# Optimization experiments

Measured on AMD Instinct MI355X. Metric: run time of the kernel, lower is better.

## Reference

```python
import jax, jax.numpy as jnp
import numpy as np

N_NODES = 100000
N_EDGES = 1600000
D_IN = 128
D_HID = 128
N_LAYERS = 3


def setup_inputs() -> dict:
    key = jax.random.key(0)
    ks = jax.random.split(key, 7)
    x = jax.random.normal(ks[0], (N_NODES, D_IN), dtype=jnp.float32)
    edge_index = jax.random.randint(ks[1], (2, N_EDGES), 0, N_NODES, dtype=jnp.int32)
    s = 1.0 / np.sqrt(D_HID)
    # stacked per-layer MLP params: lin1 (in->h), lin2 (h->h); in==h==128 for all layers
    W1 = jax.random.uniform(ks[2], (N_LAYERS, D_IN, D_HID), jnp.float32, -s, s)
    b1 = jax.random.uniform(ks[3], (N_LAYERS, D_HID), jnp.float32, -s, s)
    W2 = jax.random.uniform(ks[4], (N_LAYERS, D_HID, D_HID), jnp.float32, -s, s)
    b2 = jax.random.uniform(ks[5], (N_LAYERS, D_HID), jnp.float32, -s, s)
    return {"x": x, "edge_index": edge_index, "W1": W1, "b1": b1, "W2": W2, "b2": b2}


def _gin_layer(x, src, dst, W1, b1, W2, b2):
    # GINConv: out = MLP((1+eps)*x + sum_{j in N(i)} x_j), eps = 0
    agg = jax.ops.segment_sum(x[src], dst, num_segments=N_NODES)  # [N, C]
    h = x + agg
    h = jnp.maximum(h @ W1 + b1, 0.0)  # MLP internal ReLU
    return h @ W2 + b2


def reference(x, edge_index, W1, b1, W2, b2):
    src, dst = edge_index[0], edge_index[1]
    for i in range(N_LAYERS):
        x = _gin_layer(x, src, dst, W1[i], b1[i], W2[i], b2[i])
        if i < N_LAYERS - 1:  # inter-layer act (norm=Identity, dropout=0)
            x = jnp.maximum(x, 0.0)
    return x
```

## Files before the change

kernel.cpp:

```cpp
#include <hip/hip_runtime.h>
#include <hip/hip_bf16.h>

#define D 128
#define DD (128 * 128)

typedef float f32x4 __attribute__((ext_vector_type(4)));
typedef __bf16 bf16x8 __attribute__((ext_vector_type(8)));

__device__ __forceinline__ unsigned short f2bf(float f) {
  unsigned int u = __float_as_uint(f);
  u += 0x7fff + ((u >> 16) & 1);
  return (unsigned short)(u >> 16);
}

__device__ __forceinline__ void gl_lds16(const void* g, void* l) {
  __builtin_amdgcn_global_load_lds(
      (const __attribute__((address_space(1))) unsigned int*)g,
      (__attribute__((address_space(3))) unsigned int*)l, 16, 0, 0);
}

__device__ __forceinline__ int wave_incl_scan(int v, int lane) {
#pragma unroll
  for (int d = 1; d < 64; d <<= 1) {
    int t = __shfl_up(v, d);
    if (lane >= d) v += t;
  }
  return v;
}

#define NBK 196
#define CHUNK 4096

__global__ __launch_bounds__(256) void k_bhistP(const int* __restrict__ dst, int E,
                                                int* __restrict__ bcount, int CBn,
                                                const float* __restrict__ W1,
                                                const float* __restrict__ W2,
                                                unsigned short* __restrict__ Wt) {
  __shared__ int cnt[NBK];
  if ((int)blockIdx.x >= CBn) {
    int b = (int)blockIdx.x - CBn;
    const float* W = (b & 1) ? (W2 + (size_t)(b >> 1) * DD) : (W1 + (size_t)(b >> 1) * DD);
    unsigned short* O = Wt + (size_t)b * DD;
    for (int i = threadIdx.x; i < DD; i += 256) {
      int n = i >> 7, k = i & 127;
      O[n * D + k] = f2bf(W[k * D + n]);
    }
    return;
  }
  const int tid = threadIdx.x;
  for (int i = tid; i < NBK; i += 256) cnt[i] = 0;
  __syncthreads();
  const int e0 = blockIdx.x * CHUNK;
  const int emax = min(e0 + CHUNK, E);
  for (int e = e0 + tid; e < emax; e += 256)
    atomicAdd(&cnt[((unsigned)dst[e]) >> 9], 1);
  __syncthreads();
  for (int i = tid; i < NBK; i += 256)
    if (cnt[i]) atomicAdd(&bcount[i], cnt[i]);
}

__global__ __launch_bounds__(256) void k_binA(const int* __restrict__ src,
                                              const int* __restrict__ dst, int E,
                                              const int* __restrict__ bcount,
                                              int* __restrict__ bcursor,
                                              int* __restrict__ pairbuf) {
  __shared__ int cnt[NBK];
  __shared__ int base[NBK];
  __shared__ int bb[NBK];
  __shared__ int ws4[4];
  const int tid = threadIdx.x;
  const int e0 = blockIdx.x * CHUNK;
  const int emax = min(e0 + CHUNK, E);
  for (int i = tid; i < NBK; i += 256) cnt[i] = 0;
  {
    int lane = tid & 63, w = tid >> 6;
    int v = (tid < NBK) ? bcount[tid] : 0;
    int s = wave_incl_scan(v, lane);
    if (lane == 63) ws4[w] = s;
    __syncthreads();
    if (tid < NBK) {
      int off = 0;
      for (int k = 0; k < w; k++) off += ws4[k];
      bb[tid] = off + s - v;
    }
  }
  __syncthreads();
  for (int e = e0 + tid; e < emax; e += 256)
    atomicAdd(&cnt[((unsigned)dst[e]) >> 9], 1);
  __syncthreads();
  for (int i = tid; i < NBK; i += 256) {
    int c = cnt[i];
    int b = 0;
    if (c) b = atomicAdd(&bcursor[i], c) + bb[i];
    base[i] = b;
    cnt[i] = 0;
  }
  __syncthreads();
  for (int e = e0 + tid; e < emax; e += 256) {
    int d = dst[e];
    int bk = ((unsigned)d) >> 9;
    int pos = base[bk] + atomicAdd(&cnt[bk], 1);
    pairbuf[pos] = (src[e] << 9) | (d & 511);
  }
}

#define SEG_CAP 12800
__global__ __launch_bounds__(256) void k_binB(const int* __restrict__ pairbuf,
                                              const int* __restrict__ bcount,
                                              int* __restrict__ col,
                                              int* __restrict__ row_ptr, int N) {
  __shared__ int sdeg[512];
  __shared__ int rpl[512];
  __shared__ int cur[512];
  __shared__ int wsum[4];
  __shared__ int wsum2[4];
  __shared__ int stage[SEG_CAP];
  const int tid = threadIdx.x;
  const int lane = tid & 63, wid = tid >> 6;
  const int node0 = blockIdx.x << 9;
  const int nn = min(512, N - node0);
  {
    int vv = (tid < (int)blockIdx.x) ? bcount[tid] : 0;
    vv += __shfl_down(vv, 32); vv += __shfl_down(vv, 16);
    vv += __shfl_down(vv, 8);  vv += __shfl_down(vv, 4);
    vv += __shfl_down(vv, 2);  vv += __shfl_down(vv, 1);
    if (lane == 0) wsum2[wid] = vv;
  }
  for (int i = tid; i < 512; i += 256) { sdeg[i] = 0; cur[i] = 0; }
  __syncthreads();
  const int start = wsum2[0] + wsum2[1] + wsum2[2] + wsum2[3];
  const int end = start + bcount[blockIdx.x];
  const int sz = end - start;
  for (int i = tid; i < sz; i += 256)
    atomicAdd(&sdeg[pairbuf[start + i] & 511], 1);
  __syncthreads();
  int a = sdeg[2 * tid], b = sdeg[2 * tid + 1];
  int v = a + b;
  int s = wave_incl_scan(v, lane);
  if (lane == 63) wsum[wid] = s;
  __syncthreads();
  int off = 0;
  for (int k = 0; k < wid; k++) off += wsum[k];
  int e0l = off + s - v;
  rpl[2 * tid] = e0l;
  rpl[2 * tid + 1] = e0l + a;
  __syncthreads();
  for (int i = tid; i < nn; i += 256) row_ptr[node0 + i] = start + rpl[i];
  if (blockIdx.x == gridDim.x - 1 && tid == 0) row_ptr[N] = end;
  for (int i = tid; i < sz; i += 256) {
    int pk = pairbuf[start + i];
    int d = pk & 511;
    int pos = rpl[d] + atomicAdd(&cur[d], 1);
    if (pos < SEG_CAP) stage[pos] = (int)(((unsigned)pk) >> 9);
  }
  __syncthreads();
  for (int i = tid; i < sz; i += 256) col[start + i] = stage[i];
}

__global__ __launch_bounds__(256) void k_agg(const unsigned short* __restrict__ Y,
                                             const int* __restrict__ row_ptr,
                                             const int* __restrict__ col,
                                             const float* __restrict__ bias,
                                             unsigned short* __restrict__ H, int N) {
  int wid = (blockIdx.x * 256 + threadIdx.x) >> 6;
  int lane = threadIdx.x & 63;
  if (wid >= N) return;
  const unsigned int* Yu = (const unsigned int*)Y;
  unsigned int sv = Yu[(size_t)wid * 64 + lane];
  float2 bv = ((const float2*)bias)[lane];
  float ax = bv.x + __uint_as_float(sv << 16);
  float ay = bv.y + __uint_as_float(sv & 0xffff0000u);
  int rs = row_ptr[wid], re = row_ptr[wid + 1];
  int dcap = min(re - rs, 64);
  int cv = (lane < dcap) ? col[rs + lane] : 0;
  int j = 0;
  for (; j + 8 <= dcap; j += 8) {
    int s0 = __shfl(cv, j + 0), s1 = __shfl(cv, j + 1);
    int s2 = __shfl(cv, j + 2), s3 = __shfl(cv, j + 3);
    int s4 = __shfl(cv, j + 4), s5 = __shfl(cv, j + 5);
    int s6 = __shfl(cv, j + 6), s7 = __shfl(cv, j + 7);
    unsigned int v0 = Yu[(size_t)s0 * 64 + lane];
    unsigned int v1 = Yu[(size_t)s1 * 64 + lane];
    unsigned int v2 = Yu[(size_t)s2 * 64 + lane];
    unsigned int v3 = Yu[(size_t)s3 * 64 + lane];
    unsigned int v4 = Yu[(size_t)s4 * 64 + lane];
    unsigned int v5 = Yu[(size_t)s5 * 64 + lane];
    unsigned int v6 = Yu[(size_t)s6 * 64 + lane];
    unsigned int v7 = Yu[(size_t)s7 * 64 + lane];
    ax += ((__uint_as_float(v0 << 16) + __uint_as_float(v1 << 16)) +
           (__uint_as_float(v2 << 16) + __uint_as_float(v3 << 16))) +
          ((__uint_as_float(v4 << 16) + __uint_as_float(v5 << 16)) +
           (__uint_as_float(v6 << 16) + __uint_as_float(v7 << 16)));
    ay += ((__uint_as_float(v0 & 0xffff0000u) + __uint_as_float(v1 & 0xffff0000u)) +
           (__uint_as_float(v2 & 0xffff0000u) + __uint_as_float(v3 & 0xffff0000u))) +
          ((__uint_as_float(v4 & 0xffff0000u) + __uint_as_float(v5 & 0xffff0000u)) +
           (__uint_as_float(v6 & 0xffff0000u) + __uint_as_float(v7 & 0xffff0000u)));
  }
  for (; j < dcap; j++) {
    int s = __shfl(cv, j);
    unsigned int v = Yu[(size_t)s * 64 + lane];
    ax += __uint_as_float(v << 16);
    ay += __uint_as_float(v & 0xffff0000u);
  }
  for (int t = rs + 64; t < re; t++) {
    unsigned int v = Yu[(size_t)col[t] * 64 + lane];
    ax += __uint_as_float(v << 16);
    ay += __uint_as_float(v & 0xffff0000u);
  }
  ax = fmaxf(ax, 0.f);
  ay = fmaxf(ay, 0.f);
  ((unsigned int*)H)[(size_t)wid * 64 + lane] =
      ((unsigned int)f2bf(ay) << 16) | f2bf(ax);
}

template <bool A_FP32, bool OUT_FP32>
__global__ __launch_bounds__(256) void k_gemm(const void* __restrict__ Ain,
                                              const unsigned short* __restrict__ Wt,
                                              const float* __restrict__ bias,
                                              void* __restrict__ Cout, int M, int relu) {
  __shared__ __align__(16) unsigned short As[64 * 128];
  __shared__ __align__(16) unsigned short Bs[128 * 128];
  const int tid = threadIdx.x;
  const int wid = tid >> 6, lane = tid & 63;
  const int R0 = blockIdx.x * 64;

#pragma unroll
  for (int g = 0; g < 8; g++) {
    int flat = g * 256 + tid;
    int n = flat >> 4, p = flat & 15;
    int l = p ^ (n & 15);
    gl_lds16(Wt + (size_t)n * D + l * 8, &Bs[(size_t)(g * 256 + wid * 64) * 8]);
  }
  if (A_FP32) {
    const float* A = (const float*)Ain;
#pragma unroll
    for (int g = 0; g < 4; g++) {
      int flat = g * 256 + tid;
      int row = flat >> 4, p = flat & 15;
      int l = p ^ (row & 15);
      float4 a0 = make_float4(0.f, 0.f, 0.f, 0.f), a1 = a0;
      if (R0 + row < M) {
        a0 = *(const float4*)(A + (size_t)(R0 + row) * D + l * 8);
        a1 = *(const float4*)(A + (size_t)(R0 + row) * D + l * 8 + 4);
      }
      ushort4 v0, v1;
      v0.x = f2bf(a0.x); v0.y = f2bf(a0.y); v0.z = f2bf(a0.z); v0.w = f2bf(a0.w);
      v1.x = f2bf(a1.x); v1.y = f2bf(a1.y); v1.z = f2bf(a1.z); v1.w = f2bf(a1.w);
      *(ushort4*)&As[row * D + p * 8] = v0;
      *(ushort4*)&As[row * D + p * 8 + 4] = v1;
    }
  } else {
    const unsigned short* A = (const unsigned short*)Ain;
#pragma unroll
    for (int g = 0; g < 4; g++) {
      int flat = g * 256 + tid;
      int row = flat >> 4, p = flat & 15;
      int l = p ^ (row & 15);
      gl_lds16(A + (size_t)(R0 + row) * D + l * 8, &As[(size_t)(g * 256 + wid * 64) * 8]);
    }
  }
  __syncthreads();

  const int wr = wid >> 1, wc = wid & 1;
  const int lm = lane & 15, lq = lane >> 4;
  f32x4 acc[2][4];
#pragma unroll
  for (int i = 0; i < 2; i++)
#pragma unroll
    for (int j = 0; j < 4; j++) acc[i][j] = f32x4{0.f, 0.f, 0.f, 0.f};

#pragma unroll
  for (int kc = 0; kc < 4; kc++) {
    const int pc = (kc * 4 + lq) ^ lm;
    bf16x8 af[2], bfr[4];
#pragma unroll
    for (int i = 0; i < 2; i++)
      af[i] = *(const bf16x8*)&As[(wr * 32 + i * 16 + lm) * D + pc * 8];
#pragma unroll
    for (int j = 0; j < 4; j++)
      bfr[j] = *(const bf16x8*)&Bs[(wc * 64 + j * 16 + lm) * D + pc * 8];
#pragma unroll
    for (int i = 0; i < 2; i++)
#pragma unroll
      for (int j = 0; j < 4; j++)
        acc[i][j] = __builtin_amdgcn_mfma_f32_16x16x32_bf16(af[i], bfr[j], acc[i][j], 0, 0, 0);
  }

  float bv[4];
#pragma unroll
  for (int j = 0; j < 4; j++) bv[j] = bias ? bias[wc * 64 + j * 16 + lm] : 0.f;
#pragma unroll
  for (int i = 0; i < 2; i++) {
#pragma unroll
    for (int reg = 0; reg < 4; reg++) {
      const int gr = R0 + wr * 32 + i * 16 + lq * 4 + reg;
      if (gr < M) {
#pragma unroll
        for (int j = 0; j < 4; j++) {
          const int gc = wc * 64 + j * 16 + lm;
          float v = acc[i][j][reg] + bv[j];
          if (relu) v = fmaxf(v, 0.f);
          if (OUT_FP32)
            ((float*)Cout)[(size_t)gr * D + gc] = v;
          else
            ((unsigned short*)Cout)[(size_t)gr * D + gc] = f2bf(v);
        }
      }
    }
  }
}

__global__ __launch_bounds__(256) void k_gemm2(const unsigned short* __restrict__ Ain,
                                               const unsigned short* __restrict__ W2t,
                                               const unsigned short* __restrict__ W1t,
                                               const float* __restrict__ b2,
                                               unsigned short* __restrict__ Cout, int M) {
  __shared__ __align__(16) unsigned short As[64 * 128];
  __shared__ __align__(16) unsigned short Bs[128 * 128];
  const int tid = threadIdx.x;
  const int wid = tid >> 6, lane = tid & 63;
  const int R0 = blockIdx.x * 64;

#pragma unroll
  for (int g = 0; g < 8; g++) {
    int flat = g * 256 + tid;
    int n = flat >> 4, p = flat & 15;
    int l = p ^ (n & 15);
    gl_lds16(W2t + (size_t)n * D + l * 8, &Bs[(size_t)(g * 256 + wid * 64) * 8]);
  }
#pragma unroll
  for (int g = 0; g < 4; g++) {
    int flat = g * 256 + tid;
    int row = flat >> 4, p = flat & 15;
    int l = p ^ (row & 15);
    gl_lds16(Ain + (size_t)(R0 + row) * D + l * 8, &As[(size_t)(g * 256 + wid * 64) * 8]);
  }
  __syncthreads();

  const int wr = wid >> 1, wc = wid & 1;
  const int lm = lane & 15, lq = lane >> 4;
  f32x4 acc[2][4];
#pragma unroll
  for (int i = 0; i < 2; i++)
#pragma unroll
    for (int j = 0; j < 4; j++) acc[i][j] = f32x4{0.f, 0.f, 0.f, 0.f};
#pragma unroll
  for (int kc = 0; kc < 4; kc++) {
    const int pc = (kc * 4 + lq) ^ lm;
    bf16x8 af[2], bfr[4];
#pragma unroll
    for (int i = 0; i < 2; i++)
      af[i] = *(const bf16x8*)&As[(wr * 32 + i * 16 + lm) * D + pc * 8];
#pragma unroll
    for (int j = 0; j < 4; j++)
      bfr[j] = *(const bf16x8*)&Bs[(wc * 64 + j * 16 + lm) * D + pc * 8];
#pragma unroll
    for (int i = 0; i < 2; i++)
#pragma unroll
      for (int j = 0; j < 4; j++)
        acc[i][j] = __builtin_amdgcn_mfma_f32_16x16x32_bf16(af[i], bfr[j], acc[i][j], 0, 0, 0);
  }
  __syncthreads();

#pragma unroll
  for (int g = 0; g < 8; g++) {
    int flat = g * 256 + tid;
    int n = flat >> 4, p = flat & 15;
    int l = p ^ (n & 15);
    gl_lds16(W1t + (size_t)n * D + l * 8, &Bs[(size_t)(g * 256 + wid * 64) * 8]);
  }
  {
    float bv[4];
#pragma unroll
    for (int j = 0; j < 4; j++) bv[j] = b2[wc * 64 + j * 16 + lm];
#pragma unroll
    for (int i = 0; i < 2; i++) {
#pragma unroll
      for (int reg = 0; reg < 4; reg++) {
        const int row = wr * 32 + i * 16 + lq * 4 + reg;
#pragma unroll
        for (int j = 0; j < 4; j++) {
          const int gc = wc * 64 + j * 16 + lm;
          float v = fmaxf(acc[i][j][reg] + bv[j], 0.f);
          As[row * D + (((gc >> 3) ^ (row & 15)) << 3) + (gc & 7)] = f2bf(v);
        }
      }
    }
  }
  __syncthreads();

  f32x4 acc2[2][4];
#pragma unroll
  for (int i = 0; i < 2; i++)
#pragma unroll
    for (int j = 0; j < 4; j++) acc2[i][j] = f32x4{0.f, 0.f, 0.f, 0.f};
#pragma unroll
  for (int kc = 0; kc < 4; kc++) {
    const int pc = (kc * 4 + lq) ^ lm;
    bf16x8 af[2], bfr[4];
#pragma unroll
    for (int i = 0; i < 2; i++)
      af[i] = *(const bf16x8*)&As[(wr * 32 + i * 16 + lm) * D + pc * 8];
#pragma unroll
    for (int j = 0; j < 4; j++)
      bfr[j] = *(const bf16x8*)&Bs[(wc * 64 + j * 16 + lm) * D + pc * 8];
#pragma unroll
    for (int i = 0; i < 2; i++)
#pragma unroll
      for (int j = 0; j < 4; j++)
        acc2[i][j] = __builtin_amdgcn_mfma_f32_16x16x32_bf16(af[i], bfr[j], acc2[i][j], 0, 0, 0);
  }
#pragma unroll
  for (int i = 0; i < 2; i++) {
#pragma unroll
    for (int reg = 0; reg < 4; reg++) {
      const int gr = R0 + wr * 32 + i * 16 + lq * 4 + reg;
      if (gr < M) {
#pragma unroll
        for (int j = 0; j < 4; j++) {
          const int gc = wc * 64 + j * 16 + lm;
          Cout[(size_t)gr * D + gc] = f2bf(acc2[i][j][reg]);
        }
      }
    }
  }
}

extern "C" void kernel_launch(void* const* d_in, const int* in_sizes, int n_in,
                              void* d_out, int out_size, void* d_ws, size_t ws_size,
                              hipStream_t stream) {
  const float* x  = (const float*)d_in[0];
  const int*   ei = (const int*)d_in[1];
  const float* W1 = (const float*)d_in[2];
  const float* b1 = (const float*)d_in[3];
  const float* W2 = (const float*)d_in[4];
  const float* b2 = (const float*)d_in[5];
  const int N = in_sizes[0] / D;
  const int E = in_sizes[1] / 2;
  const int* src = ei;
  const int* dst = ei + E;

  char* ws = (char*)d_ws;
  unsigned short* Wt   = (unsigned short*)ws;
  unsigned short* bufA = Wt + 6 * DD;
  unsigned short* bufB = bufA + (size_t)(N + 1) * D;
  int* pairbuf = (int*)bufB;
  int* row_ptr = (int*)(bufB + (size_t)(N + 1) * D);
  int* colv    = row_ptr + (N + 1);
  int* bcount  = colv + E;
  int* bcursor = bcount + 256;
  float* OUT   = (float*)d_out;

  const int CB  = (E + CHUNK - 1) / CHUNK;
  const int GB  = (N + 63) / 64;
  const int AB  = (N + 3) / 4;
  const int BKB = (N + 511) / 512;

  hipMemsetAsync(bcount, 0, 512 * sizeof(int), stream);
  k_bhistP<<<CB + 6, 256, 0, stream>>>(dst, E, bcount, CB, W1, W2, Wt);
  k_binA<<<CB, 256, 0, stream>>>(src, dst, E, bcount, bcursor, pairbuf);
  k_binB<<<BKB, 256, 0, stream>>>(pairbuf, bcount, colv, row_ptr, N);

  k_gemm<true, false><<<GB, 256, 0, stream>>>(x, Wt + 0 * DD, nullptr, bufA, N, 0);
  k_agg<<<AB, 256, 0, stream>>>(bufA, row_ptr, colv, b1, bufB, N);
  k_gemm2<<<GB, 256, 0, stream>>>(bufB, Wt + 1 * DD, Wt + 2 * DD, b2, bufA, N);
  k_agg<<<AB, 256, 0, stream>>>(bufA, row_ptr, colv, b1 + D, bufB, N);
  k_gemm2<<<GB, 256, 0, stream>>>(bufB, Wt + 3 * DD, Wt + 4 * DD, b2 + D, bufA, N);
  k_agg<<<AB, 256, 0, stream>>>(bufA, row_ptr, colv, b1 + 2 * D, bufB, N);
  k_gemm<false, true><<<GB, 256, 0, stream>>>(bufB, Wt + 5 * DD, b2 + 2 * D, OUT, N, 0);
  (void)n_in; (void)out_size; (void)ws_size;
}
```

Baseline: 422.8 us.

## Split aggregation wave across two nodes and feature halves with XCD-aware block mapping

The aggregation kernel now gives each wave a pair of nodes, with each 32-lane half handling one node. Each wave covers only one 64-feature half of the row. The block index is remapped so the two feature halves of the same node pairs land on different groups of four consecutive block IDs, presumably to spread them across XCDs or L2 slices. The aim is to shorten per-wave gather chains and improve latency hiding and cache locality. In exchange, each gather now moves 128B segments instead of 256B, and imbalanced degrees within a pair leave lanes idle.

```diff
diff --git a/kernel.cpp b/kernel.cpp
--- a/kernel.cpp
+++ b/kernel.cpp
@@ -162,55 +162,78 @@
                                              const int* __restrict__ col,
                                              const float* __restrict__ bias,
                                              unsigned short* __restrict__ H, int N) {
-  int wid = (blockIdx.x * 256 + threadIdx.x) >> 6;
-  int lane = threadIdx.x & 63;
-  if (wid >= N) return;
+  const int P = (N + 1) >> 1;
+  const int bid = blockIdx.x;
+  const int x8 = bid & 7;
+  const int h = (x8 >= 4);
+  const int rank = ((bid >> 3) << 2) + (x8 & 3);
+  const int wid = threadIdx.x >> 6, lane = threadIdx.x & 63;
+  const int pair = (rank << 2) + wid;
+  if (pair >= P) return;
+  const int nA = pair << 1;
+  const bool hasB = (nA + 1 < N);
+  const int ln = lane & 31;
+  const int off = (h << 5) + ln;
+  const int grp = lane >> 5;
+  const int node = nA + grp;
+
   const unsigned int* Yu = (const unsigned int*)Y;
-  unsigned int sv = Yu[(size_t)wid * 64 + lane];
-  float2 bv = ((const float2*)bias)[lane];
+  const bool nodeOk = (node < N);
+  unsigned int sv = nodeOk ? Yu[(size_t)node * 64 + off] : 0u;
+  float2 bv = ((const float2*)bias)[off];
   float ax = bv.x + __uint_as_float(sv << 16);
   float ay = bv.y + __uint_as_float(sv & 0xffff0000u);
-  int rs = row_ptr[wid], re = row_ptr[wid + 1];
-  int dcap = min(re - rs, 64);
-  int cv = (lane < dcap) ? col[rs + lane] : 0;
+
+  int rsA = row_ptr[nA];
+  int reA = row_ptr[nA + 1];
+  int reB = hasB ? row_ptr[nA + 2] : reA;
+  rsA = __builtin_amdgcn_readfirstlane(rsA);
+  reA = __builtin_amdgcn_readfirstlane(reA);
+  reB = __builtin_amdgcn_readfirstlane(reB);
+  const int degA = reA - rsA, degB = reB - reA;
+  const int dcapA = min(degA, 32), dcapB = min(degB, 32);
+  const int myrs = grp ? reA : rsA;
+  const int mydcap = grp ? dcapB : dcapA;
+  const int maxcap = max(dcapA, dcapB);
+
+  int cv = (ln < mydcap) ? col[myrs + ln] : 0;
+
   int j = 0;
-  for (; j + 8 <= dcap; j += 8) {
-    int s0 = __shfl(cv, j + 0), s1 = __shfl(cv, j + 1);
-    int s2 = __shfl(cv, j + 2), s3 = __shfl(cv, j + 3);
-    int s4 = __shfl(cv, j + 4), s5 = __shfl(cv, j + 5);
-    int s6 = __shfl(cv, j + 6), s7 = __shfl(cv, j + 7);
-    unsigned int v0 = Yu[(size_t)s0 * 64 + lane];
-    unsigned int v1 = Yu[(size_t)s1 * 64 + lane];
-    unsigned int v2 = Yu[(size_t)s2 * 64 + lane];
-    unsigned int v3 = Yu[(size_t)s3 * 64 + lane];
-    unsigned int v4 = Yu[(size_t)s4 * 64 + lane];
-    unsigned int v5 = Yu[(size_t)s5 * 64 + lane];
-    unsigned int v6 = Yu[(size_t)s6 * 64 + lane];
-    unsigned int v7 = Yu[(size_t)s7 * 64 + lane];
-    ax += ((__uint_as_float(v0 << 16) + __uint_as_float(v1 << 16)) +
-           (__uint_as_float(v2 << 16) + __uint_as_float(v3 << 16))) +
-          ((__uint_as_float(v4 << 16) + __uint_as_float(v5 << 16)) +
-           (__uint_as_float(v6 << 16) + __uint_as_float(v7 << 16)));
-    ay += ((__uint_as_float(v0 & 0xffff0000u) + __uint_as_float(v1 & 0xffff0000u)) +
-           (__uint_as_float(v2 & 0xffff0000u) + __uint_as_float(v3 & 0xffff0000u))) +
-          ((__uint_as_float(v4 & 0xffff0000u) + __uint_as_float(v5 & 0xffff0000u)) +
-           (__uint_as_float(v6 & 0xffff0000u) + __uint_as_float(v7 & 0xffff0000u)));
-  }
-  for (; j < dcap; j++) {
-    int s = __shfl(cv, j);
-    unsigned int v = Yu[(size_t)s * 64 + lane];
+  for (; j + 8 <= maxcap; j += 8) {
+    unsigned int vv[8];
+#pragma unroll
+    for (int u = 0; u < 8; u++) {
+      int s = __shfl(cv, j + u, 32);
+      vv[u] = Yu[(size_t)s * 64 + off];
+    }
+#pragma unroll
+    for (int u = 0; u < 8; u++) {
+      if (j + u < mydcap) {
+        ax += __uint_as_float(vv[u] << 16);
+        ay += __uint_as_float(vv[u] & 0xffff0000u);
+      }
+    }
+  }
+  for (; j < maxcap; j++) {
+    int s = __shfl(cv, j, 32);
+    unsigned int v = Yu[(size_t)s * 64 + off];
+    if (j < mydcap) {
+      ax += __uint_as_float(v << 16);
+      ay += __uint_as_float(v & 0xffff0000u);
+    }
+  }
+  const int myre = grp ? reB : reA;
+  for (int t = myrs + 32; t < myre; t++) {
+    unsigned int v = Yu[(size_t)col[t] * 64 + off];
     ax += __uint_as_float(v << 16);
     ay += __uint_as_float(v & 0xffff0000u);
   }
-  for (int t = rs + 64; t < re; t++) {
-    unsigned int v = Yu[(size_t)col[t] * 64 + lane];
-    ax += __uint_as_float(v << 16);
-    ay += __uint_as_float(v & 0xffff0000u);
-  }
-  ax = fmaxf(ax, 0.f);
-  ay = fmaxf(ay, 0.f);
-  ((unsigned int*)H)[(size_t)wid * 64 + lane] =
-      ((unsigned int)f2bf(ay) << 16) | f2bf(ax);
+
+  if (nodeOk) {
+    unsigned int packed =
+        ((unsigned int)f2bf(fmaxf(ay, 0.f)) << 16) | f2bf(fmaxf(ax, 0.f));
+    ((unsigned int*)H)[(size_t)node * 64 + off] = packed;
+  }
 }
 
 template <bool A_FP32, bool OUT_FP32>
@@ -453,8 +476,9 @@
 
   const int CB  = (E + CHUNK - 1) / CHUNK;
   const int GB  = (N + 63) / 64;
-  const int AB  = (N + 3) / 4;
   const int BKB = (N + 511) / 512;
+  const int P   = (N + 1) / 2;
+  const int NB2 = ((2 * ((P + 3) / 4)) + 7) & ~7;
 
   hipMemsetAsync(bcount, 0, 512 * sizeof(int), stream);
   k_bhistP<<<CB + 6, 256, 0, stream>>>(dst, E, bcount, CB, W1, W2, Wt);
@@ -462,11 +486,11 @@
   k_binB<<<BKB, 256, 0, stream>>>(pairbuf, bcount, colv, row_ptr, N);
 
   k_gemm<true, false><<<GB, 256, 0, stream>>>(x, Wt + 0 * DD, nullptr, bufA, N, 0);
-  k_agg<<<AB, 256, 0, stream>>>(bufA, row_ptr, colv, b1, bufB, N);
+  k_agg<<<NB2, 256, 0, stream>>>(bufA, row_ptr, colv, b1, bufB, N);
   k_gemm2<<<GB, 256, 0, stream>>>(bufB, Wt + 1 * DD, Wt + 2 * DD, b2, bufA, N);
-  k_agg<<<AB, 256, 0, stream>>>(bufA, row_ptr, colv, b1 + D, bufB, N);
+  k_agg<<<NB2, 256, 0, stream>>>(bufA, row_ptr, colv, b1 + D, bufB, N);
   k_gemm2<<<GB, 256, 0, stream>>>(bufB, Wt + 3 * DD, Wt + 4 * DD, b2 + D, bufA, N);
-  k_agg<<<AB, 256, 0, stream>>>(bufA, row_ptr, colv, b1 + 2 * D, bufB, N);
+  k_agg<<<NB2, 256, 0, stream>>>(bufA, row_ptr, colv, b1 + 2 * D, bufB, N);
   k_gemm<false, true><<<GB, 256, 0, stream>>>(bufB, Wt + 5 * DD, b2 + 2 * D, OUT, N, 0);
   (void)n_in; (void)out_size; (void)ws_size;
 }
```

Measured after the change: 423.7 us. About the same (+0.2%).
